# Kernel tuning notes

Hardware: AMD Instinct MI355X
Metric: run time of the kernel (lower is better)

## Reference

```python
import jax, jax.numpy as jnp
import numpy as np

B, N, ND_, FEAT, WV = 32, 1024, 8, 2048, 300
E, T, STEPS = 20000, 2, 5
NDIM = N * ND_  # 8192


def setup_inputs() -> dict:
    key = jax.random.key(0)
    ks = jax.random.split(key, 20)
    s = 0.02
    inputs = jax.random.normal(ks[0], (B, FEAT), jnp.float32)
    wordvecs = jax.random.normal(ks[1], (N, WV), jnp.float32)
    # unique edges per type (disjoint across types) so the scatter has no duplicate indices
    rng = np.random.default_rng(0)
    codes = rng.permutation(N * N)[: T * E].reshape(T, E)
    edge_u = (codes // N).astype(np.int32)
    edge_v = (codes % N).astype(np.int32)
    ki = np.repeat(np.arange(ND_), ND_)
    kj = np.tile(np.arange(ND_), ND_)
    mat_u = (edge_u.reshape(-1)[:, None] * ND_ + ki[None, :]).reshape(-1).astype(np.int32)
    mat_v = (edge_v.reshape(-1)[:, None] * ND_ + kj[None, :]).reshape(-1).astype(np.int32)
    p = {
        'inputs': inputs, 'wordvecs': wordvecs,
        'edge_u': jnp.asarray(edge_u), 'edge_v': jnp.asarray(edge_v),
        'mat_u': jnp.asarray(mat_u), 'mat_v': jnp.asarray(mat_v),
        # Inputnet: Linear(feat+wv -> 512), Linear(512 -> node_dim)
        'W_in1': jax.random.normal(ks[2], (512, FEAT + WV), jnp.float32) * s,
        'b_in1': jnp.zeros((512,), jnp.float32),
        'W_in2': jax.random.normal(ks[3], (ND_, 512), jnp.float32) * s,
        'b_in2': jnp.zeros((ND_,), jnp.float32),
        # embnet: Linear(wv -> 50)
        'W_emb': jax.random.normal(ks[4], (50, WV), jnp.float32) * s,
        'b_emb': jnp.zeros((50,), jnp.float32),
        # relnets: one (50, 50*nd^2) matrix per edge type
        'rel_mats': jax.random.normal(ks[5], (T, 50, 50 * ND_ * ND_), jnp.float32) * s,
        # GRUCell(node_dim, node_dim)
        'W_ih': jax.random.normal(ks[6], (3 * ND_, ND_), jnp.float32) * s,
        'W_hh': jax.random.normal(ks[7], (3 * ND_, ND_), jnp.float32) * s,
        'b_ih': jnp.zeros((3 * ND_,), jnp.float32),
        'b_hh': jnp.zeros((3 * ND_,), jnp.float32),
        # outnet: Linear(nd -> 20), ReLU, Linear(20 -> 1)
        'W_o1': jax.random.normal(ks[8], (20, ND_), jnp.float32) * s,
        'b_o1': jnp.zeros((20,), jnp.float32),
        'W_o2': jax.random.normal(ks[9], (1, 20), jnp.float32) * s,
        'b_o2': jnp.zeros((1,), jnp.float32),
    }
    return p


def reference(inputs, wordvecs, edge_u, edge_v, mat_u, mat_v,
              W_in1, b_in1, W_in2, b_in2, W_emb, b_emb, rel_mats,
              W_ih, W_hh, b_ih, b_hh, W_o1, b_o1, W_o2, b_o2):
    nd = W_in2.shape[0]
    n_nodes = wordvecs.shape[0]
    ndim = n_nodes * nd
    bsz = inputs.shape[0]

    # Inputnet: per-(image, node) feature -> initial hidden state [B, N*nd]
    f = jnp.concatenate([
        jnp.broadcast_to(inputs[:, None, :], (bsz, n_nodes, inputs.shape[1])),
        jnp.broadcast_to(wordvecs[None, :, :], (bsz, n_nodes, wordvecs.shape[1])),
    ], axis=-1).reshape(bsz * n_nodes, -1)
    h = jax.nn.relu(f @ W_in1.T + b_in1) @ W_in2.T + b_in2  # [B*N, nd]
    hidden = h.reshape(bsz, ndim)

    # edge weights via Relnet per edge type
    embs = wordvecs @ W_emb.T + b_emb  # [N, 50]
    ws = []
    for t in range(rel_mats.shape[0]):
        ue = embs[edge_u[t]]  # [E, 50]
        ve = embs[edge_v[t]]  # [E, 50]
        tmp = (ue @ rel_mats[t]).reshape(ue.shape[0], embs.shape[1], nd * nd)
        ws.append(jnp.einsum('ed,edk->ek', ve, tmp))  # [E, nd^2]
    weights = jnp.concatenate(ws, axis=0).reshape(-1)

    # scatter into dense propagation matrix
    P = jnp.zeros((ndim, ndim), jnp.float32).at[mat_u, mat_v].set(weights)
    norm = jnp.sqrt(jnp.sum(P * P, axis=1))  # row L2 norms [ndim]
    norm = norm + (norm == 0).astype(P.dtype)
    P = P / norm  # NOTE: torch broadcasting divides COLUMNS by row norms (faithful)

    def gru(x, hc):
        gi = x @ W_ih.T + b_ih
        gh = hc @ W_hh.T + b_hh
        ir, iz, inn = jnp.split(gi, 3, axis=-1)
        hr, hz, hn = jnp.split(gh, 3, axis=-1)
        r = jax.nn.sigmoid(ir + hr)
        z = jax.nn.sigmoid(iz + hz)
        n = jnp.tanh(inn + r * hn)
        return (1.0 - z) * n + z * hc

    hiddens = [hidden]
    for _ in range(STEPS):
        x = jnp.tanh(hidden @ P.T)  # [B, ndim]
        hidden = gru(x.reshape(-1, nd), hidden.reshape(-1, nd)).reshape(bsz, ndim)
        hiddens.append(hidden)
    states = jnp.stack(hiddens, axis=1)  # [B, STEPS+1, ndim]

    o = jax.nn.relu(states.reshape(-1, nd) @ W_o1.T + b_o1) @ W_o2.T + b_o2  # [B*(S+1)*N, 1]
    logits = o.reshape(bsz, STEPS + 1, n_nodes).transpose(0, 2, 1)  # [B, N, S+1]
    return logits
```

## Files before the change

### kernel.cpp

```cpp
#include <hip/hip_runtime.h>
#include <math.h>

constexpr int B = 32, N = 1024, ND = 8, FEAT = 2048, WVD = 300;
constexpr int E = 20000, T = 2, STEPS = 5;
constexpr int NDIM = N * ND;
constexpr int H1 = 512;
constexpr int W1C = FEAT + WVD;
constexpr int EMB = 50;
constexpr int RC = EMB * ND * ND;
constexpr int SEG = 16;
constexpr int SEGLEN = E / SEG;

constexpr int G_KA   = 64;
constexpr int G_W1T  = 16 * 10;
constexpr int G_EMB  = N * EMB / 4;
constexpr int G_SEGH = T * N * SEG / 4;
constexpr int F1_TOT = G_KA + G_W1T + G_EMB + G_SEGH;

constexpr int G_WV2  = 256;
constexpr int G_AHAT = 13 * (N / 32) * T;
constexpr int F2_TOT = 1 + G_WV2 + G_AHAT;

constexpr int F4_TOT = 2 * N;

__global__ __launch_bounds__(256) void k_f1(
        const int* eu, int* segcnt,
        const float* inp, const float* W1, float* AbT, float* W1T,
        const float* wv, const float* We, const float* be,
        float* embs, float* embsT) {
    __shared__ float smem[8 * 260];
    int tid = threadIdx.x;
    int blk = blockIdx.x;
    if (blk < G_KA) {
        int c = tid & 7, b = tid >> 3;
        int c0 = blk * 8;
        float acc = 0.f;
        for (int kt = 0; kt < FEAT; kt += 256) {
            __syncthreads();
            {
                int r = tid >> 5, cb = (tid & 31) * 8;
                const float* src = W1 + (size_t)(c0 + r) * W1C + kt + cb;
                float4 a0 = *(const float4*)src;
                float4 a1 = *(const float4*)(src + 4);
                *(float4*)&smem[r * 260 + cb] = a0;
                *(float4*)&smem[r * 260 + cb + 4] = a1;
            }
            __syncthreads();
            const float* xr = inp + (size_t)b * FEAT + kt;
#pragma unroll 8
            for (int k4 = 0; k4 < 64; k4++) {
                float4 x = *(const float4*)(xr + k4 * 4);
                float4 w = *(const float4*)&smem[c * 260 + k4 * 4];
                acc += x.x * w.x + x.y * w.y + x.z * w.z + x.w * w.w;
            }
        }
        AbT[(c0 + c) * B + b] = acc;
    } else if (blk < G_KA + G_W1T) {
        int lb = blk - G_KA;
        int c0 = (lb % 16) * 32, k0 = (lb / 16) * 32;
        float (*tile)[33] = (float(*)[33])smem;
        int kl = tid & 31, cl4 = tid >> 5;
#pragma unroll
        for (int p = 0; p < 4; p++) {
            int c = cl4 + p * 8;
            int k = k0 + kl;
            if (k < WVD) tile[c][kl] = W1[(size_t)(c0 + c) * W1C + FEAT + k];
        }
        __syncthreads();
        int cl = tid & 31, kl4 = tid >> 5;
#pragma unroll
        for (int p = 0; p < 4; p++) {
            int kk = kl4 + p * 8;
            int k = k0 + kk;
            if (k < WVD) W1T[(size_t)k * H1 + c0 + cl] = tile[cl][kk];
        }
    } else if (blk < G_KA + G_W1T + G_EMB) {
        int lb = blk - G_KA - G_W1T;
        int wid = lb * 4 + (tid >> 6);
        int lane = tid & 63;
        int n = wid / EMB, c = wid - n * EMB;
        const float* xr = wv + (size_t)n * WVD;
        const float* wr = We + (size_t)c * WVD;
        float acc = 0.f;
#pragma unroll
        for (int i = 0; i < 5; i++) {
            int k = i * 64 + lane;
            if (k < WVD) acc += xr[k] * wr[k];
        }
        for (int m = 32; m; m >>= 1) acc += __shfl_xor(acc, m, 64);
        if (lane == 0) {
            float v = acc + be[c];
            embs[n * EMB + c] = v;
            embsT[c * N + n] = v;
        }
    } else {
        int lb = blk - G_KA - G_W1T - G_EMB;
        int wid = lb * 4 + (tid >> 6);
        int lane = tid & 63;
        int t = wid >> 14, u = (wid >> 4) & (N - 1), seg = wid & (SEG - 1);
        const int* eut = eu + t * E;
        int e0 = seg * SEGLEN, e1 = e0 + SEGLEN, cnt = 0;
        for (int c = e0; c < e1; c += 64) {
            int e = c + lane;
            bool ok = (e < e1) && (eut[e] == u);
            cnt += __popcll(__ballot(ok));
        }
        if (lane == 0) segcnt[wid] = cnt;
    }
}

__global__ __launch_bounds__(256) void k_f2(
        const int* segcnt, int* segoff, int* counts, int* ptr,
        const float* wv, const float* W1T, float* Wvb,
        const float* embsT, const float* RMbase, float* Ahat) {
    __shared__ float smemf[4096];
    int tid = threadIdx.x, blk = blockIdx.x;
    if (blk == 0) {
        int* sc = (int*)smemf;
        for (int row = tid; row < 2048; row += 256) {
            int acc = 0;
            const int* src = segcnt + row * SEG;
            int* dst = segoff + row * SEG;
#pragma unroll
            for (int s = 0; s < SEG; s++) { dst[s] = acc; acc += src[s]; }
            counts[row] = acc;
            sc[row] = acc;
        }
        __syncthreads();
        int* src = sc; int* dst = sc + 2048;
        for (int st = 1; st < 2048; st <<= 1) {
            for (int j = tid; j < 2048; j += 256)
                dst[j] = src[j] + (j >= st ? src[j - st] : 0);
            __syncthreads();
            int* tmp = src; src = dst; dst = tmp;
        }
        for (int j = tid; j < 2048; j += 256)
            ptr[j] = j ? src[j - 1] : 0;
    } else if (blk <= G_WV2) {
        int lb = blk - 1;
        int c = (lb & 1) * 256 + tid;
        int n0 = (lb >> 1) * 8;
        float (*el)[WVD] = (float(*)[WVD])smemf;
        for (int idx = tid; idx < 8 * WVD; idx += 256)
            el[idx / WVD][idx % WVD] = wv[(size_t)(n0 + idx / WVD) * WVD + idx % WVD];
        __syncthreads();
        float acc[8] = {};
        for (int k = 0; k < WVD; k++) {
            float r = W1T[(size_t)k * H1 + c];
#pragma unroll
            for (int j = 0; j < 8; j++) acc[j] += el[j][k] * r;
        }
#pragma unroll
        for (int j = 0; j < 8; j++) Wvb[(size_t)(n0 + j) * H1 + c] = acc[j];
    } else {
        int lb = blk - 1 - G_WV2;
        int t = lb / (13 * 32), r = lb % (13 * 32);
        int bx = r % 13, by = r / 13;
        const float* RM = RMbase + (size_t)t * EMB * RC;
        float* Ah = Ahat + (size_t)t * N * RC;
        int n0 = by * 32;
        int m = bx * 256 + tid;
        if (m < RC) {
            float acc[32] = {};
#pragma unroll 5
            for (int c = 0; c < EMB; c++) {
                float rr = RM[(size_t)c * RC + m];
                const float* ep = embsT + c * N + n0;
#pragma unroll
                for (int j = 0; j < 32; j++) acc[j] += ep[j] * rr;
            }
#pragma unroll
            for (int j = 0; j < 32; j++) Ah[(size_t)(n0 + j) * RC + m] = acc[j];
        }
    }
}

__global__ __launch_bounds__(256) void k_f3(
        const int* eu, const int* ev, const int* ptr, const int* segoff, int* sv) {
    int tid = threadIdx.x, blk = blockIdx.x;
    int wid = blk * 4 + (tid >> 6);
    int lane = tid & 63;
    int t = wid >> 14, u = (wid >> 4) & (N - 1), seg = wid & (SEG - 1);
    const int* eut = eu + t * E;
    const int* evt = ev + t * E;
    int row = t * N + u;
    int base = ptr[row] + segoff[row * SEG + seg];
    int e0 = seg * SEGLEN, e1 = e0 + SEGLEN, cnt = 0;
    for (int c = e0; c < e1; c += 64) {
        int e = c + lane;
        bool ok = (e < e1) && (eut[e] == u);
        unsigned long long m = __ballot(ok);
        if (ok) {
            int rank = __popcll(m & ((1ull << lane) - 1));
            sv[base + cnt + rank] = evt[e];
        }
        cnt += __popcll(m);
    }
}

__global__ __launch_bounds__(256) void k_f4(
        const int* ptr, const int* counts, const int* sv,
        const float* embs, const float* Ahat, float* wbuf, float* inorm,
        const float* AbT, const float* Wvb, const float* b1,
        const float* W2, const float* b2, float* sT0) {
    __shared__ float smem[6656];
    int tid = threadIdx.x;
    int blk = blockIdx.x;
    if (blk < N) {
        float* AL = smem;
        int u = blk;
        int wv_ = tid >> 6, k = tid & 63;
        float ssq = 0.f;
        for (int t = 0; t < T; t++) {
            __syncthreads();
            for (int idx = tid; idx < RC; idx += 256)
                AL[idx] = Ahat[((size_t)t * N + u) * RC + idx];
            __syncthreads();
            int base = ptr[t * N + u], cnt = counts[t * N + u];
            for (int i = wv_; i < cnt; i += 4) {
                int slot = base + i;
                int v = sv[slot];
                const float* vr = embs + v * EMB;
                float acc = 0.f;
#pragma unroll 10
                for (int d = 0; d < EMB; d++) acc += vr[d] * AL[d * 64 + k];
                wbuf[(size_t)slot * 64 + k] = acc;
                ssq += acc * acc;
            }
        }
        __syncthreads();
        AL[wv_ * 64 + k] = ssq;
        __syncthreads();
        if (tid < 64) {
            float tot = AL[tid] + AL[64 + tid] + AL[128 + tid] + AL[192 + tid];
            tot += __shfl_xor(tot, 1, 64);
            tot += __shfl_xor(tot, 2, 64);
            tot += __shfl_xor(tot, 4, 64);
            int ki = tid >> 3, kj = tid & 7;
            if (kj == 0) {
                float nv = sqrtf(tot);
                if (nv == 0.f) nv = 1.f;
                inorm[u * ND + ki] = 1.0f / nv;
            }
        }
    } else {
        int n = blk - N;
        float* w2s  = smem;
        float* wvs  = smem + 4096;
        float* part = smem + 4608;
        for (int idx = tid; idx < 8 * H1; idx += 256) w2s[idx] = W2[idx];
        for (int idx = tid; idx < H1; idx += 256)
            wvs[idx] = Wvb[(size_t)n * H1 + idx] + b1[idx];
        __syncthreads();
        int b = tid & 31, s = tid >> 5;
        float acc[8] = {};
        for (int i = 0; i < 64; i++) {
            int c = s * 64 + i;
            float tv = fmaxf(AbT[c * 32 + b] + wvs[c], 0.f);
#pragma unroll
            for (int ki = 0; ki < 8; ki++) acc[ki] += tv * w2s[ki * H1 + c];
        }
#pragma unroll
        for (int ki = 0; ki < 8; ki++) part[s * 256 + ki * 32 + b] = acc[ki];
        __syncthreads();
        int ki2 = tid >> 5, b2i = tid & 31;
        float tot = b2[ki2];
#pragma unroll
        for (int s2 = 0; s2 < 8; s2++) tot += part[s2 * 256 + ki2 * 32 + b2i];
        sT0[(size_t)n * 256 + tid] = tot;
    }
}

__global__ __launch_bounds__(256) void k_step(
        const int* ptr, const int* counts, const int* sv,
        const float* wbuf, const float* inorm, const float* sT, int s,
        const float* W_ih, const float* W_hh, const float* b_ih, const float* b_hh,
        const float* Wo1, const float* bo1, const float* Wo2, const float* bo2,
        float* sOut, float* out, int last) {
    __shared__ float xs[256], hs[256], hfin[256];
    __shared__ float wih[192], whh[192];
    __shared__ float w1s[160], b1s[20], w2s[20];
    __shared__ float res[8][33];
    int tid = threadIdx.x;
    int u = blockIdx.x;
    int ki = tid >> 5, b = tid & 31;
    if (tid < 192) { wih[tid] = W_ih[tid]; whh[tid] = W_hh[tid]; }
    if (last) {
        if (tid < 160) w1s[tid] = Wo1[tid];
        if (tid < 20) { b1s[tid] = bo1[tid]; w2s[tid] = Wo2[tid]; }
    }
    const float* sIn = sT + (size_t)s * NDIM * B;
    float hown = sIn[((size_t)u * 8 + ki) * B + b];
    float acc = 0.f;
    for (int t = 0; t < T; t++) {
        int base = ptr[t * N + u], cnt = counts[t * N + u];
        for (int i = 0; i < cnt; i++) {
            int slot = base + i;
            int v = sv[slot];
            const float* wp = wbuf + (size_t)slot * 64 + ki * 8;
            float4 wa = *(const float4*)wp;
            float4 wb = *(const float4*)(wp + 4);
            const float* ip = inorm + v * ND;
            const float* hp = sIn + (size_t)v * 256 + b;
            acc += (wa.x * ip[0]) * hp[0]
                 + (wa.y * ip[1]) * hp[32]
                 + (wa.z * ip[2]) * hp[64]
                 + (wa.w * ip[3]) * hp[96]
                 + (wb.x * ip[4]) * hp[128]
                 + (wb.y * ip[5]) * hp[160]
                 + (wb.z * ip[6]) * hp[192]
                 + (wb.w * ip[7]) * hp[224];
        }
    }
    float xv = tanhf(acc);
    xs[ki * 32 + b] = xv;
    hs[ki * 32 + b] = hown;
    __syncthreads();
    float gr = b_ih[ki], gz = b_ih[8 + ki], gn = b_ih[16 + ki];
    float hr = b_hh[ki], hz = b_hh[8 + ki], hn = b_hh[16 + ki];
#pragma unroll
    for (int j = 0; j < 8; j++) {
        float xj = xs[j * 32 + b], hj = hs[j * 32 + b];
        gr += wih[ki * 8 + j] * xj;
        gz += wih[(8 + ki) * 8 + j] * xj;
        gn += wih[(16 + ki) * 8 + j] * xj;
        hr += whh[ki * 8 + j] * hj;
        hz += whh[(8 + ki) * 8 + j] * hj;
        hn += whh[(16 + ki) * 8 + j] * hj;
    }
    float r = 1.f / (1.f + expf(-(gr + hr)));
    float z = 1.f / (1.f + expf(-(gz + hz)));
    float nn = tanhf(gn + r * hn);
    float hnew = (1.f - z) * nn + z * hown;
    if (!last) {
        sOut[((size_t)u * 8 + ki) * B + b] = hnew;
        return;
    }
    hfin[ki * 32 + b] = hnew;
    __syncthreads();
    int s6 = tid >> 5, bb = tid & 31;
    if (s6 < 6) {
        float x[8];
#pragma unroll
        for (int kk = 0; kk < 8; kk++)
            x[kk] = (s6 < STEPS)
                ? sT[((size_t)s6 * NDIM + u * 8 + kk) * B + bb]
                : hfin[kk * 32 + bb];
        float accv = bo2[0];
#pragma unroll
        for (int j = 0; j < 20; j++) {
            float h = b1s[j];
#pragma unroll
            for (int kk = 0; kk < 8; kk++) h += w1s[j * 8 + kk] * x[kk];
            h = fmaxf(h, 0.f);
            accv += w2s[j] * h;
        }
        res[s6][bb] = accv;
    }
    __syncthreads();
    if (tid < 192) {
        int b_w = tid / 6, s_w = tid - b_w * 6;
        out[(size_t)b_w * ((STEPS + 1) * N) + u * (STEPS + 1) + s_w] = res[s_w][b_w];
    }
}

extern "C" void kernel_launch(void* const* d_in, const int* in_sizes, int n_in,
                              void* d_out, int out_size, void* d_ws, size_t ws_size,
                              hipStream_t stream) {
    const float* inputs   = (const float*)d_in[0];
    const float* wordvecs = (const float*)d_in[1];
    const int*   edge_u   = (const int*)d_in[2];
    const int*   edge_v   = (const int*)d_in[3];
    const float* W_in1 = (const float*)d_in[6];
    const float* b_in1 = (const float*)d_in[7];
    const float* W_in2 = (const float*)d_in[8];
    const float* b_in2 = (const float*)d_in[9];
    const float* W_emb = (const float*)d_in[10];
    const float* b_emb = (const float*)d_in[11];
    const float* rel_mats = (const float*)d_in[12];
    const float* W_ih = (const float*)d_in[13];
    const float* W_hh = (const float*)d_in[14];
    const float* b_ih = (const float*)d_in[15];
    const float* b_hh = (const float*)d_in[16];
    const float* W_o1 = (const float*)d_in[17];
    const float* b_o1 = (const float*)d_in[18];
    const float* W_o2 = (const float*)d_in[19];
    const float* b_o2 = (const float*)d_in[20];
    float* out = (float*)d_out;

    char* ws = (char*)d_ws;
    size_t off = 0;
    auto alloc = [&](size_t bytes) -> void* {
        void* p = ws + off;
        off = (off + bytes + 255) & ~(size_t)255;
        return p;
    };
    int* segcnt    = (int*)alloc((size_t)T * N * SEG * 4);
    int* segoff    = (int*)alloc((size_t)T * N * SEG * 4);
    int* counts    = (int*)alloc(2048 * 4);
    int* ptr       = (int*)alloc(2048 * 4);
    int* sv        = (int*)alloc((size_t)T * E * 4);
    float* inorm   = (float*)alloc((size_t)NDIM * 4);
    float* AbT     = (float*)alloc((size_t)H1 * B * 4);
    float* W1T     = (float*)alloc((size_t)WVD * H1 * 4);
    float* Wvb     = (float*)alloc((size_t)N * H1 * 4);
    float* embs    = (float*)alloc((size_t)N * EMB * 4);
    float* embsT   = (float*)alloc((size_t)EMB * N * 4);
    float* Ahat    = (float*)alloc((size_t)T * N * RC * 4);
    float* wbuf    = (float*)alloc((size_t)T * E * 64 * 4);
    float* sT      = (float*)alloc((size_t)(STEPS + 1) * NDIM * B * 4);

    k_f1<<<F1_TOT, 256, 0, stream>>>(edge_u, segcnt, inputs, W_in1, AbT, W1T,
                                     wordvecs, W_emb, b_emb, embs, embsT);
    k_f2<<<F2_TOT, 256, 0, stream>>>(segcnt, segoff, counts, ptr,
                                     wordvecs, W1T, Wvb, embsT, rel_mats, Ahat);
    k_f3<<<T * N * SEG / 4, 256, 0, stream>>>(edge_u, edge_v, ptr, segoff, sv);
    k_f4<<<F4_TOT, 256, 0, stream>>>(ptr, counts, sv, embs, Ahat, wbuf, inorm,
                                     AbT, Wvb, b_in1, W_in2, b_in2, sT);

    for (int s = 0; s < STEPS; s++) {
        int last = (s == STEPS - 1) ? 1 : 0;
        k_step<<<N, 256, 0, stream>>>(ptr, counts, sv, wbuf, inorm, sT, s,
                                      W_ih, W_hh, b_ih, b_hh,
                                      W_o1, b_o1, W_o2, b_o2,
                                      sT + (size_t)(s + 1) * NDIM * B, out, last);
    }
}
```

Baseline: 276.5 us.

## Split-K the input GEMM and register-tile the relation-matrix product

The input-layer GEMM in k_f1 now splits its K dimension across 8 block groups (512 blocks instead of 64), writing partial sums that a new reduction branch in k_f2 adds into AbT. Separately, the Ahat computation stages the embedding slice in shared memory and has each thread compute an 8x4 register tile with float4 loads and stores, replacing 32 scalar accumulators per thread. The aim is more parallelism on the long serial K loop and better reuse and vectorization in the rel-matrix product. The cost is an extra partial-sum buffer and reduction pass.

```diff
diff --git a/kernel.cpp b/kernel.cpp
--- a/kernel.cpp
+++ b/kernel.cpp
@@ -11,21 +11,22 @@
 constexpr int SEG = 16;
 constexpr int SEGLEN = E / SEG;
 
-constexpr int G_KA   = 64;
+constexpr int G_KA   = 512;
 constexpr int G_W1T  = 16 * 10;
 constexpr int G_EMB  = N * EMB / 4;
 constexpr int G_SEGH = T * N * SEG / 4;
 constexpr int F1_TOT = G_KA + G_W1T + G_EMB + G_SEGH;
 
+constexpr int G_ARED = 8;
 constexpr int G_WV2  = 256;
 constexpr int G_AHAT = 13 * (N / 32) * T;
-constexpr int F2_TOT = 1 + G_WV2 + G_AHAT;
+constexpr int F2_TOT = 1 + G_ARED + G_WV2 + G_AHAT;
 
 constexpr int F4_TOT = 2 * N;
 
 __global__ __launch_bounds__(256) void k_f1(
         const int* eu, int* segcnt,
-        const float* inp, const float* W1, float* AbT, float* W1T,
+        const float* inp, const float* W1, float* partA, float* W1T,
         const float* wv, const float* We, const float* be,
         float* embs, float* embsT) {
     __shared__ float smem[8 * 260];
@@ -33,28 +34,27 @@
     int blk = blockIdx.x;
     if (blk < G_KA) {
         int c = tid & 7, b = tid >> 3;
-        int c0 = blk * 8;
+        int c0 = (blk & 63) * 8;
+        int ks = blk >> 6;
+        int kt = ks * 256;
+        {
+            int r = tid >> 5, cb = (tid & 31) * 8;
+            const float* src = W1 + (size_t)(c0 + r) * W1C + kt + cb;
+            float4 a0 = *(const float4*)src;
+            float4 a1 = *(const float4*)(src + 4);
+            *(float4*)&smem[r * 260 + cb] = a0;
+            *(float4*)&smem[r * 260 + cb + 4] = a1;
+        }
+        __syncthreads();
+        const float* xr = inp + (size_t)b * FEAT + kt;
         float acc = 0.f;
-        for (int kt = 0; kt < FEAT; kt += 256) {
-            __syncthreads();
-            {
-                int r = tid >> 5, cb = (tid & 31) * 8;
-                const float* src = W1 + (size_t)(c0 + r) * W1C + kt + cb;
-                float4 a0 = *(const float4*)src;
-                float4 a1 = *(const float4*)(src + 4);
-                *(float4*)&smem[r * 260 + cb] = a0;
-                *(float4*)&smem[r * 260 + cb + 4] = a1;
-            }
-            __syncthreads();
-            const float* xr = inp + (size_t)b * FEAT + kt;
 #pragma unroll 8
-            for (int k4 = 0; k4 < 64; k4++) {
-                float4 x = *(const float4*)(xr + k4 * 4);
-                float4 w = *(const float4*)&smem[c * 260 + k4 * 4];
-                acc += x.x * w.x + x.y * w.y + x.z * w.z + x.w * w.w;
-            }
-        }
-        AbT[(c0 + c) * B + b] = acc;
+        for (int k4 = 0; k4 < 64; k4++) {
+            float4 x = *(const float4*)(xr + k4 * 4);
+            float4 w = *(const float4*)&smem[c * 260 + k4 * 4];
+            acc += x.x * w.x + x.y * w.y + x.z * w.z + x.w * w.w;
+        }
+        partA[(size_t)ks * (H1 * B) + (c0 + c) * B + b] = acc;
     } else if (blk < G_KA + G_W1T) {
         int lb = blk - G_KA;
         int c0 = (lb % 16) * 32, k0 = (lb / 16) * 32;
@@ -111,6 +111,7 @@
 
 __global__ __launch_bounds__(256) void k_f2(
         const int* segcnt, int* segoff, int* counts, int* ptr,
+        const float* partA, float* AbT,
         const float* wv, const float* W1T, float* Wvb,
         const float* embsT, const float* RMbase, float* Ahat) {
     __shared__ float smemf[4096];
@@ -136,8 +137,23 @@
         }
         for (int j = tid; j < 2048; j += 256)
             ptr[j] = j ? src[j - 1] : 0;
-    } else if (blk <= G_WV2) {
-        int lb = blk - 1;
+    } else if (blk <= G_ARED) {
+        int cb = (blk - 1) * 2048 + tid * 8;
+        if (cb < H1 * B) {
+            float4 s0 = {0, 0, 0, 0}, s1 = {0, 0, 0, 0};
+#pragma unroll
+            for (int ks = 0; ks < 8; ks++) {
+                const float* p = partA + (size_t)ks * (H1 * B) + cb;
+                float4 a = *(const float4*)p;
+                float4 b4 = *(const float4*)(p + 4);
+                s0.x += a.x; s0.y += a.y; s0.z += a.z; s0.w += a.w;
+                s1.x += b4.x; s1.y += b4.y; s1.z += b4.z; s1.w += b4.w;
+            }
+            *(float4*)(AbT + cb) = s0;
+            *(float4*)(AbT + cb + 4) = s1;
+        }
+    } else if (blk <= G_ARED + G_WV2) {
+        int lb = blk - 1 - G_ARED;
         int c = (lb & 1) * 256 + tid;
         int n0 = (lb >> 1) * 8;
         float (*el)[WVD] = (float(*)[WVD])smemf;
@@ -153,24 +169,38 @@
 #pragma unroll
         for (int j = 0; j < 8; j++) Wvb[(size_t)(n0 + j) * H1 + c] = acc[j];
     } else {
-        int lb = blk - 1 - G_WV2;
+        int lb = blk - 1 - G_ARED - G_WV2;
         int t = lb / (13 * 32), r = lb % (13 * 32);
         int bx = r % 13, by = r / 13;
         const float* RM = RMbase + (size_t)t * EMB * RC;
         float* Ah = Ahat + (size_t)t * N * RC;
         int n0 = by * 32;
-        int m = bx * 256 + tid;
-        if (m < RC) {
-            float acc[32] = {};
-#pragma unroll 5
+        float (*el)[36] = (float(*)[36])smemf;
+        for (int idx = tid; idx < EMB * 32; idx += 256)
+            el[idx >> 5][idx & 31] = embsT[(idx >> 5) * N + n0 + (idx & 31)];
+        __syncthreads();
+        int mi = bx * 256 + (tid & 63) * 4;
+        int ni = (tid >> 6) * 8;
+        if (mi < RC) {
+            float acc[8][4] = {};
             for (int c = 0; c < EMB; c++) {
-                float rr = RM[(size_t)c * RC + m];
-                const float* ep = embsT + c * N + n0;
-#pragma unroll
-                for (int j = 0; j < 32; j++) acc[j] += ep[j] * rr;
+                float4 rm = *(const float4*)(RM + (size_t)c * RC + mi);
+                float4 e0 = *(const float4*)&el[c][ni];
+                float4 e1 = *(const float4*)&el[c][ni + 4];
+                float ev[8] = {e0.x, e0.y, e0.z, e0.w, e1.x, e1.y, e1.z, e1.w};
+#pragma unroll
+                for (int j = 0; j < 8; j++) {
+                    acc[j][0] += ev[j] * rm.x;
+                    acc[j][1] += ev[j] * rm.y;
+                    acc[j][2] += ev[j] * rm.z;
+                    acc[j][3] += ev[j] * rm.w;
+                }
             }
 #pragma unroll
-            for (int j = 0; j < 32; j++) Ah[(size_t)(n0 + j) * RC + m] = acc[j];
+            for (int j = 0; j < 8; j++) {
+                float4 o = {acc[j][0], acc[j][1], acc[j][2], acc[j][3]};
+                *(float4*)(Ah + (size_t)(n0 + ni + j) * RC + mi) = o;
+            }
         }
     }
 }
@@ -401,6 +431,7 @@
     int* ptr       = (int*)alloc(2048 * 4);
     int* sv        = (int*)alloc((size_t)T * E * 4);
     float* inorm   = (float*)alloc((size_t)NDIM * 4);
+    float* partA   = (float*)alloc((size_t)8 * H1 * B * 4);
     float* AbT     = (float*)alloc((size_t)H1 * B * 4);
     float* W1T     = (float*)alloc((size_t)WVD * H1 * 4);
     float* Wvb     = (float*)alloc((size_t)N * H1 * 4);
@@ -410,9 +441,10 @@
     float* wbuf    = (float*)alloc((size_t)T * E * 64 * 4);
     float* sT      = (float*)alloc((size_t)(STEPS + 1) * NDIM * B * 4);
 
-    k_f1<<<F1_TOT, 256, 0, stream>>>(edge_u, segcnt, inputs, W_in1, AbT, W1T,
+    k_f1<<<F1_TOT, 256, 0, stream>>>(edge_u, segcnt, inputs, W_in1, partA, W1T,
                                      wordvecs, W_emb, b_emb, embs, embsT);
     k_f2<<<F2_TOT, 256, 0, stream>>>(segcnt, segoff, counts, ptr,
+                                     partA, AbT,
                                      wordvecs, W1T, Wvb, embsT, rel_mats, Ahat);
     k_f3<<<T * N * SEG / 4, 256, 0, stream>>>(edge_u, edge_v, ptr, segoff, sv);
     k_f4<<<F4_TOT, 256, 0, stream>>>(ptr, counts, sv, embs, Ahat, wbuf, inorm,
```

After: 274.9 us. About the same (-0.6%).
